# Kernel optimization log

Measured on AMD Instinct MI355X. Metric: run time of the kernel, lower is better.

## Reference

```python
import jax, jax.numpy as jnp
import numpy as np

EMBED_DIM = 768
HIDDEN = 768


def setup_inputs() -> dict:
    key = jax.random.key(0)
    k1, k2, k3, k4 = jax.random.split(key, 4)
    doc_embed = jax.random.normal(k1, (32, 1024, EMBED_DIM), dtype=jnp.float32)
    query_embed = jax.random.normal(k2, (32, 128, EMBED_DIM), dtype=jnp.float32)
    # nn.Linear params: weight [H, E], bias [H]
    bound = 1.0 / np.sqrt(EMBED_DIM)
    W = jax.random.uniform(k3, (HIDDEN, EMBED_DIM), minval=-bound, maxval=bound, dtype=jnp.float32)
    b = jax.random.uniform(k4, (HIDDEN,), minval=-bound, maxval=bound, dtype=jnp.float32)
    return {"doc_embed": doc_embed, "query_embed": query_embed, "W": W, "b": b}


def reference(doc_embed, query_embed, W, b):
    # shared linear projection + ReLU
    doc_o = jax.nn.relu(jnp.einsum('bde,he->bdh', doc_embed, W) + b)    # [B, Ld, H]
    query_o = jax.nn.relu(jnp.einsum('bqe,he->bqh', query_embed, W) + b)  # [B, Lq, H]
    # unscaled cross-attention scores over query positions
    scores = jnp.einsum('bdh,bqh->bdq', doc_o, query_o)  # [B, Ld, Lq]
    attn = jax.nn.softmax(scores, axis=-1)
    out = jnp.einsum('bdq,bqe->bde', attn, query_embed)  # [B, Ld, E]
    return out
```

## Files before the change

kernel.cpp:

```cpp
#include <hip/hip_runtime.h>

typedef _Float16 f16x8 __attribute__((ext_vector_type(8)));
typedef _Float16 f16x4 __attribute__((ext_vector_type(4)));
typedef float f32x4 __attribute__((ext_vector_type(4)));

#define EMB 768
#define LQ 128
#define LD 1024
#define NB 32

typedef const __attribute__((address_space(1))) char gas_char;
typedef __attribute__((address_space(3))) char las_char;

__device__ __forceinline__ void gload16(const void* g, void* l) {
    __builtin_amdgcn_global_load_lds((gas_char*)g, (las_char*)l, 16, 0, 0);
}

#define SWZ(row, ch) ((row) * 64 + ((((ch) ^ ((row) & 7))) * 8))

#define BAR() asm volatile("s_barrier" ::: "memory")
#define LGKM0() do { asm volatile("s_waitcnt lgkmcnt(0)" ::: "memory"); \
                     __builtin_amdgcn_sched_barrier(0); } while (0)
#define VMW(N) asm volatile("s_waitcnt vmcnt(" #N ")" ::: "memory")

__global__ void cvt8_kernel(const float* __restrict__ in, _Float16* __restrict__ out, int n8) {
    int i = blockIdx.x * 256 + threadIdx.x;
    if (i >= n8) return;
    const float4 a = ((const float4*)in)[2 * i];
    const float4 b = ((const float4*)in)[2 * i + 1];
    f16x8 o;
    o[0] = (_Float16)a.x; o[1] = (_Float16)a.y; o[2] = (_Float16)a.z; o[3] = (_Float16)a.w;
    o[4] = (_Float16)b.x; o[5] = (_Float16)b.y; o[6] = (_Float16)b.z; o[7] = (_Float16)b.w;
    ((f16x8*)out)[i] = o;
}

__global__ __launch_bounds__(256) void make_vt_kernel(const float* __restrict__ Q,
                                                      _Float16* __restrict__ VT) {
    __shared__ float t[64][65];
    const int tid = threadIdx.x;
    const int q0 = blockIdx.x * 64, e0 = blockIdx.y * 64, b = blockIdx.z;
    const int rr = tid >> 4, cc = (tid & 15) * 4;
#pragma unroll
    for (int i = 0; i < 4; ++i) {
        const int row = i * 16 + rr;
        const float4 v = *(const float4*)(Q + ((size_t)b * LQ + q0 + row) * EMB + e0 + cc);
        t[row][cc + 0] = v.x; t[row][cc + 1] = v.y; t[row][cc + 2] = v.z; t[row][cc + 3] = v.w;
    }
    __syncthreads();
#pragma unroll
    for (int i = 0; i < 4; ++i) {
        const int erow = i * 16 + rr;
        f16x4 v;
#pragma unroll
        for (int j = 0; j < 4; ++j) v[j] = (_Float16)t[cc + j][erow];
        *(f16x4*)(VT + ((size_t)b * EMB + e0 + erow) * LQ + q0 + cc) = v;
    }
}

__device__ __forceinline__ void stage_tile(const _Float16* g, _Float16* l, int tid) {
#pragma unroll
    for (int i = 0; i < 4; ++i) {
        const int idx = i * 256 + tid;
        const int row = idx >> 3, ch = idx & 7;
        gload16(g + (size_t)row * EMB + ((ch ^ (row & 7)) * 8), l + (size_t)idx * 8);
    }
}

__device__ __forceinline__ void stage_d64(const _Float16* g, _Float16* l, int tid) {
#pragma unroll
    for (int i = 0; i < 2; ++i) {
        const int idx = i * 256 + tid;
        const int row = idx >> 3, ch = idx & 7;
        gload16(g + (size_t)row * EMB + ((ch ^ (row & 7)) * 8), l + (size_t)idx * 8);
    }
}

__global__ __launch_bounds__(512, 2) void proj8_kernel(
    const _Float16* __restrict__ A, const _Float16* __restrict__ W16,
    const float* __restrict__ bias, _Float16* __restrict__ OUT) {
    extern __shared__ _Float16 smem[];
    const int tid = threadIdx.x, wave = tid >> 6, lane = tid & 63;
    const int lr = lane & 15, lkg = lane >> 4;
    const int wr = wave >> 2, wc = wave & 3;

    const int nwg = gridDim.x, cpx = nwg >> 3;
    const int swz = (blockIdx.x & 7) * cpx + (blockIdx.x >> 3);
    const int rowblk = swz / 3, colblk = swz - rowblk * 3;
    const int row0 = rowblk * 256, col0 = colblk * 256;

    const int r0_ = tid >> 3, c0_ = (((tid & 7) ^ (r0_ & 7)) * 8);
    const int r1_ = (512 + tid) >> 3, c1_ = ((((512 + tid) & 7) ^ (r1_ & 7)) * 8);
    const int lo0 = tid * 8, lo1 = (512 + tid) * 8;

    const _Float16* gA0 = A + (size_t)row0 * EMB;
    const _Float16* gA1 = A + (size_t)(row0 + 128) * EMB;
    const _Float16* gB0 = W16 + (size_t)col0 * EMB;
    const _Float16* gB1 = W16 + (size_t)(col0 + 128) * EMB;

#define STAGE_PAIR(g0, g1, kt, lbase) do { \
    const _Float16* s0_ = (g0) + (kt) * 64; const _Float16* s1_ = (g1) + (kt) * 64; \
    _Float16* d_ = (lbase); \
    gload16(s0_ + (size_t)r0_ * EMB + c0_, d_ + lo0); \
    gload16(s0_ + (size_t)r1_ * EMB + c1_, d_ + lo1); \
    gload16(s1_ + (size_t)r0_ * EMB + c0_, d_ + 8192 + lo0); \
    gload16(s1_ + (size_t)r1_ * EMB + c1_, d_ + 8192 + lo1); } while (0)

    f32x4 acc[8][4];
#pragma unroll
    for (int m = 0; m < 8; ++m)
#pragma unroll
        for (int n = 0; n < 4; ++n) acc[m][n] = (f32x4){0.f, 0.f, 0.f, 0.f};

    f16x8 aF[4][2], bF[4][2];
    const int bro = (wc & 1) * 64;

#define READ_A(slot, MH) do { _Float16* ab_ = smem + (slot) * 32768 + wr * 8192; \
    _Pragma("unroll") for (int mm = 0; mm < 4; ++mm) _Pragma("unroll") for (int ks = 0; ks < 2; ++ks) \
        aF[mm][ks] = *(const f16x8*)(ab_ + SWZ(((MH) * 4 + mm) * 16 + lr, ks * 4 + lkg)); } while (0)
#define READ_B(slot, NH) do { _Float16* bb_ = smem + (slot) * 32768 + 16384 + (wc >> 1) * 8192; \
    _Pragma("unroll") for (int nn = 0; nn < 2; ++nn) _Pragma("unroll") for (int ks = 0; ks < 2; ++ks) \
        bF[(NH) * 2 + nn][ks] = *(const f16x8*)(bb_ + SWZ(bro + ((NH) * 2 + nn) * 16 + lr, ks * 4 + lkg)); } while (0)
#define MFMA_Q(MH, NH) do { __builtin_amdgcn_s_setprio(1); \
    _Pragma("unroll") for (int mm = 0; mm < 4; ++mm) _Pragma("unroll") for (int nn = 0; nn < 2; ++nn) \
    _Pragma("unroll") for (int ks = 0; ks < 2; ++ks) \
        acc[(MH) * 4 + mm][(NH) * 2 + nn] = __builtin_amdgcn_mfma_f32_16x16x32_f16( \
            aF[mm][ks], bF[(NH) * 2 + nn][ks], acc[(MH) * 4 + mm][(NH) * 2 + nn], 0, 0, 0); \
    __builtin_amdgcn_s_setprio(0); } while (0)

    STAGE_PAIR(gB0, gB1, 0, smem + 16384);
    STAGE_PAIR(gA0, gA1, 0, smem);
    STAGE_PAIR(gB0, gB1, 1, smem + 32768 + 16384);
    STAGE_PAIR(gA0, gA1, 1, smem + 32768);
    VMW(8);
    BAR();

#pragma unroll 1
    for (int j = 0; j < 6; ++j) {
        const int kt2 = 2 * j + 2, kt3 = 2 * j + 3;
        READ_B(0, 0); READ_B(0, 1); READ_A(0, 0);
        BAR(); LGKM0(); MFMA_Q(0, 0); BAR();
        BAR(); LGKM0(); MFMA_Q(0, 1); BAR();
        READ_A(0, 1);
        if (j < 5) STAGE_PAIR(gB0, gB1, kt2, smem + 16384);
        BAR(); LGKM0(); MFMA_Q(1, 0); BAR();
        if (j < 5) { STAGE_PAIR(gA0, gA1, kt2, smem); VMW(4); }
        else       { VMW(0); }
        BAR(); LGKM0(); MFMA_Q(1, 1); BAR();
        READ_B(1, 0); READ_B(1, 1); READ_A(1, 0);
        BAR(); LGKM0(); MFMA_Q(0, 0); BAR();
        BAR(); LGKM0(); MFMA_Q(0, 1); BAR();
        READ_A(1, 1);
        if (j < 5) STAGE_PAIR(gB0, gB1, kt3, smem + 32768 + 16384);
        BAR(); LGKM0(); MFMA_Q(1, 0); BAR();
        if (j < 5) { STAGE_PAIR(gA0, gA1, kt3, smem + 32768); VMW(4); }
        BAR(); LGKM0(); MFMA_Q(1, 1); BAR();
    }

    const int crow = lkg * 4;
#pragma unroll
    for (int n = 0; n < 4; ++n) {
        const int gc = col0 + wc * 64 + n * 16 + lr;
        const float bv = bias[gc];
#pragma unroll
        for (int m = 0; m < 8; ++m) {
            const size_t gr = (size_t)row0 + wr * 128 + m * 16 + crow;
#pragma unroll
            for (int r = 0; r < 4; ++r) {
                float v = acc[m][n][r] + bv;
                OUT[(gr + r) * EMB + gc] = (_Float16)(v > 0.f ? v : 0.f);
            }
        }
    }
#undef STAGE_PAIR
#undef READ_A
#undef READ_B
#undef MFMA_Q
}

__global__ __launch_bounds__(256) void attn64_kernel(
    const _Float16* __restrict__ Do, const _Float16* __restrict__ Qo,
    const _Float16* __restrict__ VT, float* __restrict__ OUT) {
    __shared__ __align__(16) _Float16 smem[24576];
    const int tid = threadIdx.x, wave = tid >> 6, lane = tid & 63;
    const int lr = lane & 15, lkg = lane >> 4;

    const int l = blockIdx.x;
    const int x = l & 7, i = l >> 3;
    const int b = x * 4 + (i >> 4), dblk = i & 15;

    const _Float16* gd = Do + ((size_t)b * LD + dblk * 64) * EMB;
    const _Float16* gq = Qo + (size_t)b * LQ * EMB;

    f32x4 s[8];
#pragma unroll
    for (int n = 0; n < 8; ++n) s[n] = (f32x4){0.f, 0.f, 0.f, 0.f};

    stage_d64(gd, smem, tid);
    stage_tile(gq, smem + 4096, tid);
    int cur = 0;
    for (int it = 0; it < 12; ++it) {
        __syncthreads();
        if (it < 11) {
            stage_d64(gd + (it + 1) * 64, smem + (cur ^ 1) * 12288, tid);
            stage_tile(gq + (it + 1) * 64, smem + (cur ^ 1) * 12288 + 4096, tid);
        }
        const _Float16* sD = smem + cur * 12288;
        const _Float16* sQ = sD + 4096;
#pragma unroll
        for (int kk = 0; kk < 2; ++kk) {
            const int ch = kk * 4 + lkg;
            const f16x8 am = *(const f16x8*)(sD + SWZ(wave * 16 + lr, ch));
#pragma unroll
            for (int n = 0; n < 8; ++n) {
                const f16x8 bq = *(const f16x8*)(sQ + SWZ(n * 16 + lr, ch));
                s[n] = __builtin_amdgcn_mfma_f32_16x16x32_f16(am, bq, s[n], 0, 0, 0);
            }
        }
        cur ^= 1;
    }
    __syncthreads();

    _Float16 (*P)[136] = (_Float16 (*)[136])smem;
    const int crow = lkg * 4;
#pragma unroll
    for (int r = 0; r < 4; ++r) {
        float mx = -1e30f;
#pragma unroll
        for (int n = 0; n < 8; ++n) mx = fmaxf(mx, s[n][r]);
#pragma unroll
        for (int off = 1; off < 16; off <<= 1) mx = fmaxf(mx, __shfl_xor(mx, off));
        float p[8], sum = 0.f;
#pragma unroll
        for (int n = 0; n < 8; ++n) { p[n] = __expf(s[n][r] - mx); sum += p[n]; }
#pragma unroll
        for (int off = 1; off < 16; off <<= 1) sum += __shfl_xor(sum, off);
        const float inv = 1.f / sum;
        const int row = wave * 16 + crow + r;
#pragma unroll
        for (int n = 0; n < 8; ++n) P[row][n * 16 + lr] = (_Float16)(p[n] * inv);
    }
    __syncthreads();

    const _Float16* vtb = VT + (size_t)b * EMB * LQ;
    const size_t dbase = (size_t)b * LD + dblk * 64 + wave * 16 + crow;
#pragma unroll 1
    for (int nc = 0; nc < 6; ++nc) {
        f32x4 o[8];
#pragma unroll
        for (int t = 0; t < 8; ++t) o[t] = (f32x4){0.f, 0.f, 0.f, 0.f};
#pragma unroll
        for (int ks = 0; ks < 4; ++ks) {
            const f16x8 am = *(const f16x8*)(&P[wave * 16 + lr][ks * 32 + lkg * 8]);
#pragma unroll
            for (int t = 0; t < 8; ++t) {
                const f16x8 bv = *(const f16x8*)(vtb + (size_t)(nc * 128 + t * 16 + lr) * LQ
                                                 + ks * 32 + lkg * 8);
                o[t] = __builtin_amdgcn_mfma_f32_16x16x32_f16(am, bv, o[t], 0, 0, 0);
            }
        }
#pragma unroll
        for (int t = 0; t < 8; ++t) {
            const int e = nc * 128 + t * 16 + lr;
#pragma unroll
            for (int r = 0; r < 4; ++r)
                OUT[(dbase + r) * EMB + e] = o[t][r];
        }
    }
}

extern "C" void kernel_launch(void* const* d_in, const int* in_sizes, int n_in,
                              void* d_out, int out_size, void* d_ws, size_t ws_size,
                              hipStream_t stream) {
    const float* doc   = (const float*)d_in[0];
    const float* query = (const float*)d_in[1];
    const float* W     = (const float*)d_in[2];
    const float* bias  = (const float*)d_in[3];
    float* out = (float*)d_out;

    const size_t nW  = (size_t)EMB * EMB;
    const size_t nVT = (size_t)NB * EMB * LQ;
    const size_t nDo = (size_t)NB * LD * EMB;
    const size_t nQo = (size_t)NB * LQ * EMB;
    const size_t need = (nW + nVT + nDo + nQo) * sizeof(_Float16);
    if (ws_size < need) return;

    _Float16* W16 = (_Float16*)d_ws;
    _Float16* VT  = W16 + nW;
    _Float16* Do  = VT + nVT;
    _Float16* Qo  = Do + nDo;

    _Float16* doc16 = (_Float16*)d_out;
    _Float16* q16   = doc16 + nDo;

    cvt8_kernel<<<(int)(nDo / 8 / 256), 256, 0, stream>>>(doc, doc16, (int)(nDo / 8));
    cvt8_kernel<<<(int)(nQo / 8 / 256), 256, 0, stream>>>(query, q16, (int)(nQo / 8));
    cvt8_kernel<<<(int)(nW / 8 / 256), 256, 0, stream>>>(W, W16, (int)(nW / 8));
    make_vt_kernel<<<dim3(2, 12, NB), 256, 0, stream>>>(query, VT);

    hipFuncSetAttribute(reinterpret_cast<const void*>(&proj8_kernel),
                        hipFuncAttributeMaxDynamicSharedMemorySize, 131072);
    proj8_kernel<<<dim3(144 * 3), 512, 131072, stream>>>(doc16, W16, bias, Do);

    attn64_kernel<<<dim3(NB * 16), 256, 0, stream>>>(Do, Qo, VT, out);
}
```

Before: 150.8 us.

## Fuse fp32-to-fp16 conversion of doc and query into the projection GEMM

Removes the separate cvt8 passes over doc and query. The projection kernel now loads fp32 A tiles into registers, converts them to fp16 and writes them into swizzled LDS itself, while W still goes through async global_load_lds. This saves a full read and write of the fp16 copies, but the A path now uses register staging and LDS stores in the MFMA pipeline, which adds register pressure and lgkm waits.

```diff
diff --git a/kernel.cpp b/kernel.cpp
--- a/kernel.cpp
+++ b/kernel.cpp
@@ -22,6 +22,7 @@
 #define LGKM0() do { asm volatile("s_waitcnt lgkmcnt(0)" ::: "memory"); \
                      __builtin_amdgcn_sched_barrier(0); } while (0)
 #define VMW(N) asm volatile("s_waitcnt vmcnt(" #N ")" ::: "memory")
+#define LGKM_FLUSH() asm volatile("s_waitcnt lgkmcnt(0)" ::: "memory")
 
 __global__ void cvt8_kernel(const float* __restrict__ in, _Float16* __restrict__ out, int n8) {
     int i = blockIdx.x * 256 + threadIdx.x;
@@ -75,9 +76,10 @@
     }
 }
 
-__global__ __launch_bounds__(512, 2) void proj8_kernel(
-    const _Float16* __restrict__ A, const _Float16* __restrict__ W16,
-    const float* __restrict__ bias, _Float16* __restrict__ OUT) {
+__global__ __launch_bounds__(512, 2) void proj8f_kernel(
+    const float* __restrict__ doc, const float* __restrict__ query,
+    const _Float16* __restrict__ W16, const float* __restrict__ bias,
+    _Float16* __restrict__ OUT) {
     extern __shared__ _Float16 smem[];
     const int tid = threadIdx.x, wave = tid >> 6, lane = tid & 63;
     const int lr = lane & 15, lkg = lane >> 4;
@@ -88,17 +90,38 @@
     const int rowblk = swz / 3, colblk = swz - rowblk * 3;
     const int row0 = rowblk * 256, col0 = colblk * 256;
 
+    const float* gAf = (rowblk < 128) ? doc + (size_t)row0 * EMB
+                                      : query + (size_t)(row0 - 32768) * EMB;
+    const _Float16* gB0 = W16 + (size_t)col0 * EMB;
+    const _Float16* gB1 = W16 + (size_t)(col0 + 128) * EMB;
+
     const int r0_ = tid >> 3, c0_ = (((tid & 7) ^ (r0_ & 7)) * 8);
     const int r1_ = (512 + tid) >> 3, c1_ = ((((512 + tid) & 7) ^ (r1_ & 7)) * 8);
     const int lo0 = tid * 8, lo1 = (512 + tid) * 8;
 
-    const _Float16* gA0 = A + (size_t)row0 * EMB;
-    const _Float16* gA1 = A + (size_t)(row0 + 128) * EMB;
-    const _Float16* gB0 = W16 + (size_t)col0 * EMB;
-    const _Float16* gB1 = W16 + (size_t)(col0 + 128) * EMB;
-
-#define STAGE_PAIR(g0, g1, kt, lbase) do { \
-    const _Float16* s0_ = (g0) + (kt) * 64; const _Float16* s1_ = (g1) + (kt) * 64; \
+    int arow_[4], ach_[4];
+#pragma unroll
+    for (int w = 0; w < 4; ++w) {
+        const int c = w * 512 + tid;
+        arow_[w] = c >> 3; ach_[w] = c & 7;
+    }
+    float4 fA[4][2];
+
+#define ISSUE_A(kt) do { _Pragma("unroll") for (int w_ = 0; w_ < 4; ++w_) { \
+        const float* s_ = gAf + (size_t)arow_[w_] * EMB + (kt) * 64 + ach_[w_] * 8; \
+        fA[w_][0] = *(const float4*)s_; fA[w_][1] = *(const float4*)(s_ + 4); } } while (0)
+
+#define WRITE_A(slot) do { _Pragma("unroll") for (int w_ = 0; w_ < 4; ++w_) { \
+        f16x8 v_; \
+        v_[0] = (_Float16)fA[w_][0].x; v_[1] = (_Float16)fA[w_][0].y; \
+        v_[2] = (_Float16)fA[w_][0].z; v_[3] = (_Float16)fA[w_][0].w; \
+        v_[4] = (_Float16)fA[w_][1].x; v_[5] = (_Float16)fA[w_][1].y; \
+        v_[6] = (_Float16)fA[w_][1].z; v_[7] = (_Float16)fA[w_][1].w; \
+        *(f16x8*)(smem + (slot) * 32768 + (arow_[w_] >> 7) * 8192 \
+                  + SWZ(arow_[w_] & 127, ach_[w_])) = v_; } } while (0)
+
+#define STAGE_B(kt, lbase) do { \
+    const _Float16* s0_ = gB0 + (kt) * 64; const _Float16* s1_ = gB1 + (kt) * 64; \
     _Float16* d_ = (lbase); \
     gload16(s0_ + (size_t)r0_ * EMB + c0_, d_ + lo0); \
     gload16(s0_ + (size_t)r1_ * EMB + c1_, d_ + lo1); \
@@ -127,32 +150,36 @@
             aF[mm][ks], bF[(NH) * 2 + nn][ks], acc[(MH) * 4 + mm][(NH) * 2 + nn], 0, 0, 0); \
     __builtin_amdgcn_s_setprio(0); } while (0)
 
-    STAGE_PAIR(gB0, gB1, 0, smem + 16384);
-    STAGE_PAIR(gA0, gA1, 0, smem);
-    STAGE_PAIR(gB0, gB1, 1, smem + 32768 + 16384);
-    STAGE_PAIR(gA0, gA1, 1, smem + 32768);
-    VMW(8);
+    ISSUE_A(0);
+    STAGE_B(0, smem + 16384);
+    WRITE_A(0);
+    ISSUE_A(1);
+    STAGE_B(1, smem + 32768 + 16384);
+    WRITE_A(1);
+    LGKM_FLUSH();
     BAR();
 
 #pragma unroll 1
     for (int j = 0; j < 6; ++j) {
         const int kt2 = 2 * j + 2, kt3 = 2 * j + 3;
+        if (j < 5) ISSUE_A(kt2);
         READ_B(0, 0); READ_B(0, 1); READ_A(0, 0);
         BAR(); LGKM0(); MFMA_Q(0, 0); BAR();
         BAR(); LGKM0(); MFMA_Q(0, 1); BAR();
         READ_A(0, 1);
-        if (j < 5) STAGE_PAIR(gB0, gB1, kt2, smem + 16384);
+        if (j < 5) STAGE_B(kt2, smem + 16384);
         BAR(); LGKM0(); MFMA_Q(1, 0); BAR();
-        if (j < 5) { STAGE_PAIR(gA0, gA1, kt2, smem); VMW(4); }
+        if (j < 5) { WRITE_A(0); LGKM_FLUSH(); }
         else       { VMW(0); }
         BAR(); LGKM0(); MFMA_Q(1, 1); BAR();
+        if (j < 5) ISSUE_A(kt3);
         READ_B(1, 0); READ_B(1, 1); READ_A(1, 0);
         BAR(); LGKM0(); MFMA_Q(0, 0); BAR();
         BAR(); LGKM0(); MFMA_Q(0, 1); BAR();
         READ_A(1, 1);
-        if (j < 5) STAGE_PAIR(gB0, gB1, kt3, smem + 32768 + 16384);
+        if (j < 5) STAGE_B(kt3, smem + 32768 + 16384);
         BAR(); LGKM0(); MFMA_Q(1, 0); BAR();
-        if (j < 5) { STAGE_PAIR(gA0, gA1, kt3, smem + 32768); VMW(4); }
+        if (j < 5) { WRITE_A(1); LGKM_FLUSH(); }
         BAR(); LGKM0(); MFMA_Q(1, 1); BAR();
     }
 
@@ -171,7 +198,9 @@
             }
         }
     }
-#undef STAGE_PAIR
+#undef ISSUE_A
+#undef WRITE_A
+#undef STAGE_B
 #undef READ_A
 #undef READ_B
 #undef MFMA_Q
@@ -289,17 +318,12 @@
     _Float16* Do  = VT + nVT;
     _Float16* Qo  = Do + nDo;
 
-    _Float16* doc16 = (_Float16*)d_out;
-    _Float16* q16   = doc16 + nDo;
-
-    cvt8_kernel<<<(int)(nDo / 8 / 256), 256, 0, stream>>>(doc, doc16, (int)(nDo / 8));
-    cvt8_kernel<<<(int)(nQo / 8 / 256), 256, 0, stream>>>(query, q16, (int)(nQo / 8));
     cvt8_kernel<<<(int)(nW / 8 / 256), 256, 0, stream>>>(W, W16, (int)(nW / 8));
     make_vt_kernel<<<dim3(2, 12, NB), 256, 0, stream>>>(query, VT);
 
-    hipFuncSetAttribute(reinterpret_cast<const void*>(&proj8_kernel),
+    hipFuncSetAttribute(reinterpret_cast<const void*>(&proj8f_kernel),
                         hipFuncAttributeMaxDynamicSharedMemorySize, 131072);
-    proj8_kernel<<<dim3(144 * 3), 512, 131072, stream>>>(doc16, W16, bias, Do);
+    proj8f_kernel<<<dim3(144 * 3), 512, 131072, stream>>>(doc, query, W16, bias, Do);
 
     attn64_kernel<<<dim3(NB * 16), 256, 0, stream>>>(Do, Qo, VT, out);
 }
```

Result: slower. 164.2 us (median of 3 runs) (+8.8%).

## Merge conversion kernels and restructure attention score loop with explicit pipelining

Applied to the files above, without the earlier changes.

The three fp32-to-fp16 conversion launches are merged into one kernel that dispatches on block index, removing launch gaps. The score-accumulation loop in the attention kernel is rewritten as a manually unrolled double-buffered pipeline. It uses explicit vmcnt waits, raw barriers, register-staged LDS reads and raised wave priority around the MFMA bursts, so global loads overlap compute. This adds more barriers per iteration, and correctness depends on the vmcnt counts matching the number of outstanding loads.

```diff
diff --git a/kernel.cpp b/kernel.cpp
--- a/kernel.cpp
+++ b/kernel.cpp
@@ -23,15 +23,25 @@
                      __builtin_amdgcn_sched_barrier(0); } while (0)
 #define VMW(N) asm volatile("s_waitcnt vmcnt(" #N ")" ::: "memory")
 
-__global__ void cvt8_kernel(const float* __restrict__ in, _Float16* __restrict__ out, int n8) {
-    int i = blockIdx.x * 256 + threadIdx.x;
-    if (i >= n8) return;
-    const float4 a = ((const float4*)in)[2 * i];
-    const float4 b = ((const float4*)in)[2 * i + 1];
+#define DOCB 12288
+#define QB   1536
+#define WB   288
+__global__ void cvt_all_kernel(const float* __restrict__ doc, const float* __restrict__ query,
+                               const float* __restrict__ W, _Float16* __restrict__ doc16,
+                               _Float16* __restrict__ q16, _Float16* __restrict__ W16) {
+    const int bid = blockIdx.x;
+    const float* src;
+    _Float16* dst;
+    int i;
+    if (bid < DOCB)            { src = doc;   dst = doc16; i = bid * 256 + threadIdx.x; }
+    else if (bid < DOCB + QB)  { src = query; dst = q16;   i = (bid - DOCB) * 256 + threadIdx.x; }
+    else                       { src = W;     dst = W16;   i = (bid - DOCB - QB) * 256 + threadIdx.x; }
+    const float4 a = ((const float4*)src)[2 * i];
+    const float4 b = ((const float4*)src)[2 * i + 1];
     f16x8 o;
     o[0] = (_Float16)a.x; o[1] = (_Float16)a.y; o[2] = (_Float16)a.z; o[3] = (_Float16)a.w;
     o[4] = (_Float16)b.x; o[5] = (_Float16)b.y; o[6] = (_Float16)b.z; o[7] = (_Float16)b.w;
-    ((f16x8*)out)[i] = o;
+    ((f16x8*)dst)[i] = o;
 }
 
 __global__ __launch_bounds__(256) void make_vt_kernel(const float* __restrict__ Q,
@@ -191,33 +201,53 @@
     const _Float16* gd = Do + ((size_t)b * LD + dblk * 64) * EMB;
     const _Float16* gq = Qo + (size_t)b * LQ * EMB;
 
+#define STAGE6(kt, base) do { \
+    stage_d64(gd + (kt) * 64, (base), tid); \
+    stage_tile(gq + (kt) * 64, (base) + 4096, tid); } while (0)
+
     f32x4 s[8];
 #pragma unroll
     for (int n = 0; n < 8; ++n) s[n] = (f32x4){0.f, 0.f, 0.f, 0.f};
 
-    stage_d64(gd, smem, tid);
-    stage_tile(gq, smem + 4096, tid);
-    int cur = 0;
-    for (int it = 0; it < 12; ++it) {
-        __syncthreads();
-        if (it < 11) {
-            stage_d64(gd + (it + 1) * 64, smem + (cur ^ 1) * 12288, tid);
-            stage_tile(gq + (it + 1) * 64, smem + (cur ^ 1) * 12288 + 4096, tid);
-        }
-        const _Float16* sD = smem + cur * 12288;
-        const _Float16* sQ = sD + 4096;
-#pragma unroll
-        for (int kk = 0; kk < 2; ++kk) {
-            const int ch = kk * 4 + lkg;
-            const f16x8 am = *(const f16x8*)(sD + SWZ(wave * 16 + lr, ch));
-#pragma unroll
-            for (int n = 0; n < 8; ++n) {
-                const f16x8 bq = *(const f16x8*)(sQ + SWZ(n * 16 + lr, ch));
-                s[n] = __builtin_amdgcn_mfma_f32_16x16x32_f16(am, bq, s[n], 0, 0, 0);
-            }
-        }
-        cur ^= 1;
-    }
+    f16x8 am, bq[8];
+#define READ_KK(base, kk) do { \
+    const _Float16* sD_ = (base); const _Float16* sQ_ = (base) + 4096; \
+    const int ch_ = (kk) * 4 + lkg; \
+    am = *(const f16x8*)(sD_ + SWZ(wave * 16 + lr, ch_)); \
+    _Pragma("unroll") for (int n_ = 0; n_ < 8; ++n_) \
+        bq[n_] = *(const f16x8*)(sQ_ + SWZ(n_ * 16 + lr, ch_)); } while (0)
+#define MFMA8() do { __builtin_amdgcn_s_setprio(1); \
+    _Pragma("unroll") for (int n_ = 0; n_ < 8; ++n_) \
+        s[n_] = __builtin_amdgcn_mfma_f32_16x16x32_f16(am, bq[n_], s[n_], 0, 0, 0); \
+    __builtin_amdgcn_s_setprio(0); } while (0)
+
+    STAGE6(0, smem);
+    STAGE6(1, smem + 12288);
+
+#pragma unroll
+    for (int j = 0; j < 6; ++j) {
+        if (j > 0) STAGE6(2 * j + 1, smem + 12288);
+        VMW(6);
+        BAR();
+        READ_KK(smem, 0);
+        LGKM0(); MFMA8();
+        BAR();
+        READ_KK(smem, 1);
+        LGKM0(); MFMA8();
+        BAR();
+        if (j < 5) { STAGE6(2 * j + 2, smem); VMW(6); }
+        else       { VMW(0); }
+        BAR();
+        READ_KK(smem + 12288, 0);
+        LGKM0(); MFMA8();
+        BAR();
+        READ_KK(smem + 12288, 1);
+        LGKM0(); MFMA8();
+        BAR();
+    }
+#undef STAGE6
+#undef READ_KK
+#undef MFMA8
     __syncthreads();
 
     _Float16 (*P)[136] = (_Float16 (*)[136])smem;
@@ -250,12 +280,12 @@
         for (int t = 0; t < 8; ++t) o[t] = (f32x4){0.f, 0.f, 0.f, 0.f};
 #pragma unroll
         for (int ks = 0; ks < 4; ++ks) {
-            const f16x8 am = *(const f16x8*)(&P[wave * 16 + lr][ks * 32 + lkg * 8]);
+            const f16x8 pa = *(const f16x8*)(&P[wave * 16 + lr][ks * 32 + lkg * 8]);
 #pragma unroll
             for (int t = 0; t < 8; ++t) {
                 const f16x8 bv = *(const f16x8*)(vtb + (size_t)(nc * 128 + t * 16 + lr) * LQ
                                                  + ks * 32 + lkg * 8);
-                o[t] = __builtin_amdgcn_mfma_f32_16x16x32_f16(am, bv, o[t], 0, 0, 0);
+                o[t] = __builtin_amdgcn_mfma_f32_16x16x32_f16(pa, bv, o[t], 0, 0, 0);
             }
         }
 #pragma unroll
@@ -292,9 +322,7 @@
     _Float16* doc16 = (_Float16*)d_out;
     _Float16* q16   = doc16 + nDo;
 
-    cvt8_kernel<<<(int)(nDo / 8 / 256), 256, 0, stream>>>(doc, doc16, (int)(nDo / 8));
-    cvt8_kernel<<<(int)(nQo / 8 / 256), 256, 0, stream>>>(query, q16, (int)(nQo / 8));
-    cvt8_kernel<<<(int)(nW / 8 / 256), 256, 0, stream>>>(W, W16, (int)(nW / 8));
+    cvt_all_kernel<<<DOCB + QB + WB, 256, 0, stream>>>(doc, query, W, doc16, q16, W16);
     make_vt_kernel<<<dim3(2, 12, NB), 256, 0, stream>>>(query, VT);
 
     hipFuncSetAttribute(reinterpret_cast<const void*>(&proj8_kernel),
```

Result: faster. 147.2 us (-2.4%).
